# Kernel tuning notes

Measured on AMD Instinct MI355X. Metric: run time of the kernel, lower is better.

Reference implementation:

```python
import jax, jax.numpy as jnp
import numpy as np

# Fixed sparse pair interactions from the original module
PAIR_IDX = np.array([[0, 4], [0, 7], [0, 9], [0, 3], [1, 4], [2, 3]])  # [P=6, 2]

B, F, H, P = 524288, 10, 64, 6


def setup_inputs() -> dict:
    key = jax.random.key(0)
    ks = jax.random.split(key, 9)
    return {
        "x": jax.random.normal(ks[0], (B, F), dtype=jnp.float32),
        "raw_mean": jnp.zeros((F,), dtype=jnp.float32),
        "raw_std": jnp.ones((F,), dtype=jnp.float32),
        # Stacked FeatureNet params: Linear(1->H) weight [F,H], bias [F,H]; Linear(H->1) weight [F,H], bias [F]
        "fw1": jax.random.normal(ks[1], (F, H), dtype=jnp.float32) * 0.5,
        "fb1": jax.random.normal(ks[2], (F, H), dtype=jnp.float32) * 0.1,
        "fw2": jax.random.normal(ks[3], (F, H), dtype=jnp.float32) * 0.1,
        "fb2": jax.random.normal(ks[4], (F,), dtype=jnp.float32) * 0.1,
        # Stacked PairNet params: Linear(2->H) weight [P,2,H], bias [P,H]; Linear(H->1) weight [P,H], bias [P]
        "pw1": jax.random.normal(ks[5], (P, 2, H), dtype=jnp.float32) * 0.5,
        "pb1": jax.random.normal(ks[6], (P, H), dtype=jnp.float32) * 0.1,
        "pw2": jax.random.normal(ks[7], (P, H), dtype=jnp.float32) * 0.1,
        "pb2": jax.random.normal(ks[8], (P,), dtype=jnp.float32) * 0.1,
    }


def reference(x, raw_mean, raw_std, fw1, fb1, fw2, fb2, pw1, pb1, pw2, pb2):
    # transformed_raw_features: log-transform feature 4
    raw = x.at[:, 4].set(jnp.log(jnp.clip(x[:, 4] * 10.0, 1e-6)))
    s = (raw - raw_mean) / raw_std  # [B, F]

    # All FeatureNets as one batched pass: Linear(1->H) is an outer product
    h = jax.nn.gelu(s[:, :, None] * fw1[None, :, :] + fb1[None, :, :], approximate=False)  # [B, F, H]
    feat = jnp.einsum('bfh,fh->bf', h, fw2) + fb2  # [B, F]
    additive = feat.sum(axis=-1)  # [B]

    # All PairNets as one batched pass over the 6 fixed pairs
    sp = s[:, PAIR_IDX]  # [B, P, 2]
    hp = jax.nn.gelu(jnp.einsum('bpi,pih->bph', sp, pw1) + pb1[None, :, :], approximate=False)  # [B, P, H]
    pair = jnp.einsum('bph,ph->bp', hp, pw2) + pb2  # [B, P]
    pairwise = pair.sum(axis=-1)  # [B]

    return additive + pairwise
```

## Files before the change

### kernel.cpp

```cpp
#include <hip/hip_runtime.h>
#include <math.h>

namespace {

constexpr int F = 10;
constexpr int H = 64;
constexpr int P = 6;

constexpr int F1D = 4;
constexpr int F1D_LIST[F1D] = {4, 5, 6, 8};
constexpr int   NLUT       = 1024;
constexpr float LUT_LO     = -14.5f;
constexpr float LUT_HI     = 6.5f;
constexpr float LUT_DX     = (LUT_HI - LUT_LO) / NLUT;
constexpr float LUT_INVDX  = NLUT / (LUT_HI - LUT_LO);
constexpr float LUT_POSMAX = (float)(NLUT - 2) + 0.999f;

constexpr int NB  = 128;
constexpr int N2D = P * NB * NB;
constexpr float A_LO  = -6.5f;
constexpr float A_SPAN = 13.0f;
constexpr int PI[P] = {0, 0, 0, 0, 1, 2};
constexpr int PJ[P] = {4, 7, 9, 3, 4, 3};
constexpr float B_LO[P]   = {-14.5f, -6.5f, -6.5f, -6.5f, -14.5f, -6.5f};
constexpr float B_SPAN[P] = { 19.0f,  13.0f, 13.0f, 13.0f,  19.0f, 13.0f};
constexpr float POSMAX2   = (float)(NB - 1) - 0.001f;
constexpr int EXF[P] = {0, 7, 9, 3, 1, 2};
constexpr int EXA[P] = {0, 1, 1, 1, 0, 0};

constexpr int WS_LUT1_OFF = 4 * N2D;
constexpr int WS_FLOATS   = 4 * N2D + 2 * F1D * NLUT;
constexpr int N_ENTRIES   = N2D + F1D * NLUT;

__device__ __forceinline__ float gelu_exact(float x) {
    const float kInvSqrt2 = 0.70710678118654752440f;
    float u = x * kInvSqrt2;
    float a = fabsf(u);
    float t = __builtin_amdgcn_rcpf(fmaf(0.3275911f, a, 1.0f));
    float poly = t * fmaf(t, fmaf(t, fmaf(t, fmaf(t, 0.5307027145f,
                                                  -0.7265760135f),
                                           0.7107068705f),
                                   -0.142248368f),
                          0.127414796f);
    float e = __expf(-a * a);
    float half_erfc = poly * e;
    float m = x * half_erfc;
    return (x >= 0.0f) ? (x - m) : m;
}

__device__ __forceinline__ float feat_mlp(
    int f, float s,
    const float* __restrict__ fw1, const float* __restrict__ fb1,
    const float* __restrict__ fw2, const float* __restrict__ fb2)
{
    const float* w1 = fw1 + f * H;
    const float* b1 = fb1 + f * H;
    const float* w2 = fw2 + f * H;
    float acc = fb2[f];
    #pragma unroll 8
    for (int h = 0; h < H; ++h)
        acc = fmaf(gelu_exact(fmaf(s, w1[h], b1[h])), w2[h], acc);
    return acc;
}

__device__ __forceinline__ void build_entry(
    int idx,
    const float* __restrict__ fw1, const float* __restrict__ fb1,
    const float* __restrict__ fw2, const float* __restrict__ fb2,
    const float* __restrict__ pw1, const float* __restrict__ pb1,
    const float* __restrict__ pw2, const float* __restrict__ pb2,
    float* __restrict__ ws)
{
    if (idx < N2D) {
        const int p   = idx / (NB * NB);
        const int rem = idx - p * (NB * NB);
        const int ia  = rem >> 7;
        const int jb  = rem & (NB - 1);
        const bool f4 = (p == 0) | (p == 4);
        const float blo   = f4 ? -14.5f : -6.5f;
        const float bstep = (f4 ? 19.0f : 13.0f) / (float)(NB - 1);
        const float astep = A_SPAN / (float)(NB - 1);
        const float sa = fmaf((float)ia, astep, A_LO);
        const float sb = fmaf((float)jb, bstep, blo);
        const float* wa = pw1 + (p * 2 + 0) * H;
        const float* wb = pw1 + (p * 2 + 1) * H;
        const float* bb = pb1 + p * H;
        const float* w2 = pw2 + p * H;
        float acc = pb2[p];
        #pragma unroll 8
        for (int h = 0; h < H; ++h) {
            acc = fmaf(gelu_exact(fmaf(sa, wa[h], fmaf(sb, wb[h], bb[h]))),
                       w2[h], acc);
        }
        acc += feat_mlp(EXF[p], EXA[p] ? sb : sa, fw1, fb1, fw2, fb2);

        const int pbase = p * NB * NB;
        float* q = ws + 4 * (pbase + ia * NB + jb);
        q[0] = acc;
        if (jb > 0)           q[-4 + 1] = acc;
        if (ia > 0)           q[-4 * NB + 2] = acc;
        if (ia > 0 && jb > 0) q[-4 * (NB + 1) + 3] = acc;
    } else if (idx < N_ENTRIES) {
        const int k = idx - N2D;
        const int t = k >> 10;
        const int i = k & 1023;
        const int f = F1D_LIST[t];
        const float s = LUT_LO + (float)i * LUT_DX;
        const float acc = feat_mlp(f, s, fw1, fb1, fw2, fb2);
        ws[WS_LUT1_OFF + 2 * k] = acc;
        if (i > 0) ws[WS_LUT1_OFF + 2 * k - 1] = acc;
    }
}

__device__ __forceinline__ float bilerp4(const float4* __restrict__ lutp,
                                         float sa, float sb,
                                         float ainv, float blo, float binv) {
    float pa = fminf(fmaxf((sa - A_LO) * ainv, 0.0f), POSMAX2);
    float pb = fminf(fmaxf((sb - blo) * binv, 0.0f), POSMAX2);
    int ia = (int)pa;
    int jb = (int)pb;
    float fa = pa - (float)ia;
    float fb = pb - (float)jb;
    float4 q = lutp[ia * NB + jb];
    float v0 = fmaf(fb, q.y - q.x, q.x);
    float v1 = fmaf(fb, q.w - q.z, q.z);
    return fmaf(fa, v1 - v0, v0);
}

__global__ __launch_bounds__(256) void build_luts(
    const float* __restrict__ fw1, const float* __restrict__ fb1,
    const float* __restrict__ fw2, const float* __restrict__ fb2,
    const float* __restrict__ pw1, const float* __restrict__ pb1,
    const float* __restrict__ pw2, const float* __restrict__ pb2,
    float* __restrict__ ws)
{
    const int idx = blockIdx.x * blockDim.x + threadIdx.x;
    build_entry(idx, fw1, fb1, fw2, fb2, pw1, pb1, pw2, pb2, ws);
}

__global__ __launch_bounds__(256) void risk_lut2_kernel(
    const float* __restrict__ x,
    const float* __restrict__ raw_mean,
    const float* __restrict__ raw_std,
    const float* __restrict__ ws,
    float* __restrict__ out,
    int nrows)
{
    const float4* lut2 = reinterpret_cast<const float4*>(ws);
    const float2* lut1 = reinterpret_cast<const float2*>(ws + WS_LUT1_OFF);
    const int r = blockIdx.x * blockDim.x + threadIdx.x;
    if (r >= nrows) return;

    float v[F];
    {
        const float2* xp = reinterpret_cast<const float2*>(x + (size_t)r * F);
        float2 a = xp[0], b = xp[1], c = xp[2], d = xp[3], e = xp[4];
        v[0] = a.x; v[1] = a.y; v[2] = b.x; v[3] = b.y;
        v[4] = c.x; v[5] = c.y; v[6] = d.x; v[7] = d.y;
        v[8] = e.x; v[9] = e.y;
    }
    float s[F];
    #pragma unroll
    for (int f = 0; f < F; ++f) {
        float ra = v[f];
        if (f == 4) ra = __logf(fmaxf(ra * 10.0f, 1e-6f));
        s[f] = (ra - raw_mean[f]) / raw_std[f];
    }

    float acc = 0.0f;

    #pragma unroll
    for (int t = 0; t < F1D; ++t) {
        float pos = fminf(fmaxf(fmaf(s[F1D_LIST[t]], LUT_INVDX,
                                     -LUT_LO * LUT_INVDX), 0.0f), LUT_POSMAX);
        int i = (int)pos;
        float fr = pos - (float)i;
        float2 c = lut1[t * NLUT + i];
        acc += fmaf(fr, c.y - c.x, c.x);
    }

    constexpr float AINV = (float)(NB - 1) / A_SPAN;
    #pragma unroll
    for (int p = 0; p < P; ++p) {
        const float4* lutp = lut2 + p * NB * NB;
        const float binv = (float)(NB - 1) / B_SPAN[p];
        acc += bilerp4(lutp, s[PI[p]], s[PJ[p]], AINV, B_LO[p], binv);
    }

    out[r] = acc;
}

__global__ __launch_bounds__(256) void risk_full_kernel(
    const float* __restrict__ x,
    const float* __restrict__ raw_mean,
    const float* __restrict__ raw_std,
    const float* __restrict__ fw1,
    const float* __restrict__ fb1,
    const float* __restrict__ fw2,
    const float* __restrict__ fb2,
    const float* __restrict__ pw1,
    const float* __restrict__ pb1,
    const float* __restrict__ pw2,
    const float* __restrict__ pb2,
    float* __restrict__ out,
    int nrows)
{
    const int r = blockIdx.x * blockDim.x + threadIdx.x;
    if (r >= nrows) return;

    float s[F];
    #pragma unroll
    for (int f = 0; f < F; ++f) {
        float ra = x[(size_t)r * F + f];
        if (f == 4) ra = __logf(fmaxf(ra * 10.0f, 1e-6f));
        s[f] = (ra - raw_mean[f]) / raw_std[f];
    }
    float acc = 0.0f;
    #pragma unroll
    for (int f = 0; f < F; ++f) {
        acc += feat_mlp(f, s[f], fw1, fb1, fw2, fb2);
    }
    #pragma unroll
    for (int p = 0; p < P; ++p) {
        const float* wa = pw1 + (p * 2 + 0) * H;
        const float* wb = pw1 + (p * 2 + 1) * H;
        const float* bb = pb1 + p * H;
        const float* w2 = pw2 + p * H;
        const float xa = s[PI[p]], xb = s[PJ[p]];
        float a0 = 0.0f;
        #pragma unroll 8
        for (int h = 0; h < H; ++h)
            a0 = fmaf(gelu_exact(fmaf(xa, wa[h], fmaf(xb, wb[h], bb[h]))), w2[h], a0);
        acc += a0 + pb2[p];
    }
    out[r] = acc;
}

}

extern "C" void kernel_launch(void* const* d_in, const int* in_sizes, int n_in,
                              void* d_out, int out_size, void* d_ws, size_t ws_size,
                              hipStream_t stream)
{
    const float* x        = (const float*)d_in[0];
    const float* raw_mean = (const float*)d_in[1];
    const float* raw_std  = (const float*)d_in[2];
    const float* fw1      = (const float*)d_in[3];
    const float* fb1      = (const float*)d_in[4];
    const float* fw2      = (const float*)d_in[5];
    const float* fb2      = (const float*)d_in[6];
    const float* pw1      = (const float*)d_in[7];
    const float* pb1      = (const float*)d_in[8];
    const float* pw2      = (const float*)d_in[9];
    const float* pb2      = (const float*)d_in[10];
    float* out = (float*)d_out;

    const int nrows = in_sizes[0] / F;
    const int block = 256;
    const int grid = (nrows + block - 1) / block;

    const size_t lut_bytes = (size_t)WS_FLOATS * sizeof(float);
    if (ws_size >= lut_bytes) {
        float* ws = (float*)d_ws;
        build_luts<<<(N_ENTRIES + 255) / 256, 256, 0, stream>>>(
            fw1, fb1, fw2, fb2, pw1, pb1, pw2, pb2, ws);
        risk_lut2_kernel<<<grid, block, 0, stream>>>(
            x, raw_mean, raw_std, ws, out, nrows);
    } else {
        risk_full_kernel<<<grid, block, 0, stream>>>(
            x, raw_mean, raw_std, fw1, fb1, fw2, fb2,
            pw1, pb1, pw2, pb2, out, nrows);
    }
}
```

Baseline: 107.3 us.

## Move all per-feature 1D tables into LDS and drop folding into pair tables

Stops folding single-feature MLP contributions into the 2D pair tables and instead builds a 1D table for all ten features. The eval kernel loads these tables (40 KB) into shared memory per block and interpolates from LDS using two scalar reads. This is meant to move the 1D gathers off global/L2. The cost is a 40 KB copy per 256-row block, more interpolation work per row, and reduced occupancy from the large LDS allocation.

```diff
diff --git a/kernel.cpp b/kernel.cpp
--- a/kernel.cpp
+++ b/kernel.cpp
@@ -7,8 +7,6 @@
 constexpr int H = 64;
 constexpr int P = 6;
 
-constexpr int F1D = 4;
-constexpr int F1D_LIST[F1D] = {4, 5, 6, 8};
 constexpr int   NLUT       = 1024;
 constexpr float LUT_LO     = -14.5f;
 constexpr float LUT_HI     = 6.5f;
@@ -25,12 +23,10 @@
 constexpr float B_LO[P]   = {-14.5f, -6.5f, -6.5f, -6.5f, -14.5f, -6.5f};
 constexpr float B_SPAN[P] = { 19.0f,  13.0f, 13.0f, 13.0f,  19.0f, 13.0f};
 constexpr float POSMAX2   = (float)(NB - 1) - 0.001f;
-constexpr int EXF[P] = {0, 7, 9, 3, 1, 2};
-constexpr int EXA[P] = {0, 1, 1, 1, 0, 0};
 
 constexpr int WS_LUT1_OFF = 4 * N2D;
-constexpr int WS_FLOATS   = 4 * N2D + 2 * F1D * NLUT;
-constexpr int N_ENTRIES   = N2D + F1D * NLUT;
+constexpr int WS_FLOATS   = 4 * N2D + F * NLUT;
+constexpr int N_ENTRIES   = N2D + F * NLUT;
 
 __device__ __forceinline__ float gelu_exact(float x) {
     const float kInvSqrt2 = 0.70710678118654752440f;
@@ -92,8 +88,6 @@
             acc = fmaf(gelu_exact(fmaf(sa, wa[h], fmaf(sb, wb[h], bb[h]))),
                        w2[h], acc);
         }
-        acc += feat_mlp(EXF[p], EXA[p] ? sb : sa, fw1, fb1, fw2, fb2);
-
         const int pbase = p * NB * NB;
         float* q = ws + 4 * (pbase + ia * NB + jb);
         q[0] = acc;
@@ -102,13 +96,10 @@
         if (ia > 0 && jb > 0) q[-4 * (NB + 1) + 3] = acc;
     } else if (idx < N_ENTRIES) {
         const int k = idx - N2D;
-        const int t = k >> 10;
+        const int f = k >> 10;
         const int i = k & 1023;
-        const int f = F1D_LIST[t];
         const float s = LUT_LO + (float)i * LUT_DX;
-        const float acc = feat_mlp(f, s, fw1, fb1, fw2, fb2);
-        ws[WS_LUT1_OFF + 2 * k] = acc;
-        if (i > 0) ws[WS_LUT1_OFF + 2 * k - 1] = acc;
+        ws[WS_LUT1_OFF + k] = feat_mlp(f, s, fw1, fb1, fw2, fb2);
     }
 }
 
@@ -146,8 +137,18 @@
     float* __restrict__ out,
     int nrows)
 {
+    __shared__ float slut[F * NLUT];
     const float4* lut2 = reinterpret_cast<const float4*>(ws);
-    const float2* lut1 = reinterpret_cast<const float2*>(ws + WS_LUT1_OFF);
+
+    {
+        const float4* g = reinterpret_cast<const float4*>(ws + WS_LUT1_OFF);
+        float4* l = reinterpret_cast<float4*>(slut);
+        #pragma unroll
+        for (int i = 0; i < (F * NLUT) / 4 / 256; ++i)
+            l[threadIdx.x + i * 256] = g[threadIdx.x + i * 256];
+    }
+    __syncthreads();
+
     const int r = blockIdx.x * blockDim.x + threadIdx.x;
     if (r >= nrows) return;
 
@@ -170,13 +171,14 @@
     float acc = 0.0f;
 
     #pragma unroll
-    for (int t = 0; t < F1D; ++t) {
-        float pos = fminf(fmaxf(fmaf(s[F1D_LIST[t]], LUT_INVDX,
-                                     -LUT_LO * LUT_INVDX), 0.0f), LUT_POSMAX);
+    for (int f = 0; f < F; ++f) {
+        float pos = fminf(fmaxf(fmaf(s[f], LUT_INVDX, -LUT_LO * LUT_INVDX),
+                                0.0f), LUT_POSMAX);
         int i = (int)pos;
         float fr = pos - (float)i;
-        float2 c = lut1[t * NLUT + i];
-        acc += fmaf(fr, c.y - c.x, c.x);
+        float a = slut[f * NLUT + i];
+        float b = slut[f * NLUT + i + 1];
+        acc += fmaf(fr, b - a, a);
     }
 
     constexpr float AINV = (float)(NB - 1) / A_SPAN;
```

Measured after the change: 103.0 us. -4.0%, faster.
